# Performance work log

Measured on AMD Instinct MI355X. Metric: run time of the kernel, lower is better.

Reference implementation:

```python
import jax, jax.numpy as jnp
import numpy as np

MARGIN = 1.0


def setup_inputs() -> dict:
    key = jax.random.key(0)
    k1, k2, k3 = jax.random.split(key, 3)
    N, F = 4096, 512
    a = jax.random.normal(k1, (N, F), dtype=jnp.float32)
    b = jax.random.normal(k2, (N, F), dtype=jnp.float32)
    labels = jax.random.randint(k3, (N,), 0, 16, dtype=jnp.int32)
    return {"a": a, "b": b, "labels": labels}


def reference(a, b, labels):
    # D[i, j] = ||b_i - a_j||  (torch: Xa=a[None], Xb=b[:,None], sum over feat)
    # GEMM form of the pairwise sqdist; clamp tiny fp negatives before sqrt.
    Dsq = (jnp.sum(b * b, axis=1)[:, None]
           + jnp.sum(a * a, axis=1)[None, :]
           - 2.0 * (b @ a.T))
    D = jnp.sqrt(jnp.maximum(Dsq, 0.0))            # [N, N]
    Dexpm = jnp.exp(MARGIN - D)                    # [N, N]

    same = labels[:, None] == labels[None, :]      # [N, N]
    eye = jnp.eye(labels.shape[0], dtype=bool)
    pos_mask = same & ~eye                         # ordered positive pairs (i, j)
    neg_mask = ~same                               # negative pairs (labels differ)

    # neg_i sum for row i: sum_k Dexpm[i, k] over k with labels[k] != labels[i]
    row_negsum = jnp.sum(jnp.where(neg_mask, Dexpm, 0.0), axis=1)  # [N]

    # J_ij = log(neg_ik_sum + neg_jl_sum) + D[i, j]; hinged and squared
    J = jnp.log(row_negsum[:, None] + row_negsum[None, :]) + D
    hinge_sq = jnp.square(jnp.maximum(J, 0.0))

    num_pos = jnp.sum(pos_mask)
    return jnp.sum(jnp.where(pos_mask, hinge_sq, 0.0)) / (2.0 * num_pos)
```

## Files before the change

### kernel.cpp

```cpp
#include <hip/hip_runtime.h>
#include <math.h>

#define NROW 4096
#define FDIM 512
#define MARGIN 1.0f
#define NLAB 16
#define PREP_BLK 1024

typedef __attribute__((ext_vector_type(8))) short short8;
typedef __attribute__((ext_vector_type(4))) float floatx4;

__device__ inline unsigned short f2bf(float x) {
    unsigned u = __float_as_uint(x);
    return (unsigned short)((u + 0x7FFFu + ((u >> 16) & 1u)) >> 16);
}
__device__ inline void glds16(const unsigned short* g, unsigned short* l) {
    __builtin_amdgcn_global_load_lds(
        (const __attribute__((address_space(1))) unsigned int*)g,
        (__attribute__((address_space(3))) unsigned int*)l, 16, 0, 0);
}
#define WAIT_VM_BARRIER(N)                                          \
    do {                                                            \
        asm volatile("s_waitcnt vmcnt(" #N ")" ::: "memory");       \
        __builtin_amdgcn_s_barrier();                               \
        __builtin_amdgcn_sched_barrier(0);                          \
    } while (0)

__device__ inline float fast_sqrt_pos(float dsq) {
    float c = fmaxf(dsq, 1e-20f);
    return c * __frsqrt_rn(c);
}

__global__ __launch_bounds__(256) void prep_kernel(
    const float* __restrict__ a, const float* __restrict__ b,
    const int* __restrict__ labels,
    unsigned short* __restrict__ abf, unsigned short* __restrict__ bbf,
    float* __restrict__ na, float* __restrict__ nb,
    float* __restrict__ rns, float* __restrict__ loss,
    int* __restrict__ perm, int* __restrict__ goff,
    int* __restrict__ wl, int* __restrict__ wlmeta) {
    const int t = threadIdx.x;

    if (blockIdx.x == PREP_BLK) {
        __shared__ int hist[NLAB], off[NLAB], cur[NLAB];
        if (t < NLAB) hist[t] = 0;
        __syncthreads();
        for (int i = t; i < NROW; i += 256) atomicAdd(&hist[labels[i] & 15], 1);
        __syncthreads();
        if (t == 0) {
            int acc = 0;
            for (int g = 0; g < NLAB; ++g) { off[g] = acc; acc += hist[g]; }
            int n = 0;
            long long np = 0;
            for (int g = 0; g < NLAB; ++g) {
                goff[g] = off[g];
                int c = hist[g];
                np += (long long)c * (long long)(c - 1);
                int nt = (c + 63) >> 6;
                for (int ti = 0; ti < nt; ++ti)
                    for (int tj = 0; tj < nt; ++tj)
                        wl[n++] = (g << 12) | (ti << 6) | tj;
            }
            goff[NLAB] = NROW;
            wlmeta[0] = n;
            wlmeta[1] = (int)np;
            wlmeta[2] = 0;
            loss[0]   = 0.f;
        }
        __syncthreads();
        if (t < NLAB) cur[t] = off[t];
        __syncthreads();
        for (int i = t; i < NROW; i += 256) {
            int pos = atomicAdd(&cur[labels[i] & 15], 1);
            perm[pos] = i;
        }
        return;
    }

    const int grp = t >> 6;
    const int ln  = t & 63;
    const int row = blockIdx.x * 4 + grp;
    const float4* a4 = (const float4*)(a + (size_t)row * FDIM);
    const float4* b4 = (const float4*)(b + (size_t)row * FDIM);
    const int f = ln * 2;
    float4 va0 = a4[f], va1 = a4[f + 1];
    float4 vb0 = b4[f], vb1 = b4[f + 1];
    float sa = va0.x * va0.x + va0.y * va0.y + va0.z * va0.z + va0.w * va0.w
             + va1.x * va1.x + va1.y * va1.y + va1.z * va1.z + va1.w * va1.w;
    float sb = vb0.x * vb0.x + vb0.y * vb0.y + vb0.z * vb0.z + vb0.w * vb0.w
             + vb1.x * vb1.x + vb1.y * vb1.y + vb1.z * vb1.z + vb1.w * vb1.w;
    short8 ua, ub;
    ua[0] = (short)f2bf(va0.x); ua[1] = (short)f2bf(va0.y);
    ua[2] = (short)f2bf(va0.z); ua[3] = (short)f2bf(va0.w);
    ua[4] = (short)f2bf(va1.x); ua[5] = (short)f2bf(va1.y);
    ua[6] = (short)f2bf(va1.z); ua[7] = (short)f2bf(va1.w);
    ub[0] = (short)f2bf(vb0.x); ub[1] = (short)f2bf(vb0.y);
    ub[2] = (short)f2bf(vb0.z); ub[3] = (short)f2bf(vb0.w);
    ub[4] = (short)f2bf(vb1.x); ub[5] = (short)f2bf(vb1.y);
    ub[6] = (short)f2bf(vb1.z); ub[7] = (short)f2bf(vb1.w);
    *(short8*)&abf[(size_t)row * FDIM + (size_t)f * 4] = ua;
    *(short8*)&bbf[(size_t)row * FDIM + (size_t)f * 4] = ub;
    #pragma unroll
    for (int o = 32; o > 0; o >>= 1) {
        sa += __shfl_down(sa, o);
        sb += __shfl_down(sb, o);
    }
    if (ln == 0) {
        na[row] = sa;
        nb[row] = sb;
        rns[row] = 0.f;
    }
}

__global__ __launch_bounds__(1024, 4) void pass_neg(
    const unsigned short* __restrict__ abf, const unsigned short* __restrict__ bbf,
    const int* __restrict__ labels,
    const float* __restrict__ na, const float* __restrict__ nb,
    float* __restrict__ rns)
{
    __shared__ __align__(16) unsigned short arena[65536];
    __shared__ float rpart[4][256];

    const int t    = threadIdx.x;
    const int lane = t & 63;
    const int w    = t >> 6;
    const int wi   = w >> 2;
    const int wj   = w & 3;
    const int lr   = lane & 15;
    const int lq   = lane >> 4;

    const int bid = blockIdx.x;
    const int wg  = (bid & 7) * 32 + (bid >> 3);
    const int by  = wg >> 4, bx = wg & 15;
    const int ti  = by * 256;
    const int tj  = bx * 256;

    floatx4 acc[4][4];
    #pragma unroll
    for (int i = 0; i < 4; ++i)
        #pragma unroll
        for (int j = 0; j < 4; ++j)
            acc[i][j] = (floatx4){0.f, 0.f, 0.f, 0.f};

    const int srow = t >> 2;
    const int sqs  = (t & 3) ^ ((srow >> 1) & 3);
    const unsigned offA = (unsigned)(tj + srow) * FDIM + sqs * 8;
    const unsigned offB = (unsigned)(ti + srow) * FDIM + sqs * 8;

    auto stage = [&](int s) {
        unsigned short* As = arena + (s & 3) * 16384;
        unsigned short* Bs = As + 8192;
        const int kk = s * 32;
        glds16(abf + offA + kk, As + t * 8);
        glds16(bbf + offB + kk, Bs + t * 8);
    };

    stage(0);
    stage(1);
    stage(2);
    WAIT_VM_BARRIER(4);

    #pragma unroll
    for (int it = 0; it < 16; ++it) {
        if (it < 13) stage(it + 3);

        const unsigned short* As = arena + (it & 3) * 16384;
        const unsigned short* Bs = As + 8192;
        short8 af[4], bv[4];
        #pragma unroll
        for (int ri = 0; ri < 4; ++ri) {
            int R = wi * 64 + ri * 16 + lr;
            af[ri] = *(const short8*)
                &Bs[R * 32 + ((lq ^ ((R >> 1) & 3))) * 8];
        }
        #pragma unroll
        for (int rj = 0; rj < 4; ++rj) {
            int R = wj * 64 + rj * 16 + lr;
            bv[rj] = *(const short8*)
                &As[R * 32 + ((lq ^ ((R >> 1) & 3))) * 8];
        }
        __builtin_amdgcn_s_setprio(1);
        #pragma unroll
        for (int ri = 0; ri < 4; ++ri)
            #pragma unroll
            for (int rj = 0; rj < 4; ++rj)
                acc[ri][rj] = __builtin_amdgcn_mfma_f32_16x16x32_bf16(
                    af[ri], bv[rj], acc[ri][rj], 0, 0, 0);
        __builtin_amdgcn_s_setprio(0);

        if (it < 13) {
            WAIT_VM_BARRIER(4);
        } else if (it == 13) {
            WAIT_VM_BARRIER(2);
        } else if (it == 14) {
            WAIT_VM_BARRIER(0);
        }
    }

    int   ljv[4]; float najv[4];
    #pragma unroll
    for (int rj = 0; rj < 4; ++rj) {
        int jl = wj * 64 + rj * 16 + lr;
        ljv[rj]  = labels[tj + jl];
        najv[rj] = na[tj + jl];
    }
    #pragma unroll
    for (int ri = 0; ri < 4; ++ri) {
        float rs[4] = {0.f, 0.f, 0.f, 0.f};
        int liv[4]; float nbv[4];
        #pragma unroll
        for (int r = 0; r < 4; ++r) {
            int il = wi * 64 + ri * 16 + lq * 4 + r;
            liv[r] = labels[ti + il];
            nbv[r] = nb[ti + il];
        }
        #pragma unroll
        for (int rj = 0; rj < 4; ++rj)
            #pragma unroll
            for (int r = 0; r < 4; ++r) {
                float dsq  = nbv[r] + najv[rj] - 2.f * acc[ri][rj][r];
                float D    = fast_sqrt_pos(dsq);
                float mask = (liv[r] != ljv[rj]) ? 1.f : 0.f;
                rs[r] = fmaf(mask, __expf(MARGIN - D), rs[r]);
            }
        #pragma unroll
        for (int r = 0; r < 4; ++r) {
            #pragma unroll
            for (int o = 8; o > 0; o >>= 1) rs[r] += __shfl_down(rs[r], o, 16);
        }
        if (lr == 0) {
            #pragma unroll
            for (int r = 0; r < 4; ++r)
                rpart[wj][wi * 64 + ri * 16 + lq * 4 + r] = rs[r];
        }
    }
    __syncthreads();
    if (t < 256) {
        float s = rpart[0][t] + rpart[1][t] + rpart[2][t] + rpart[3][t];
        atomicAdd(&rns[ti + t], s);
    }
}

__global__ __launch_bounds__(512) void pass2_pos(
    const unsigned short* __restrict__ abf, const unsigned short* __restrict__ bbf,
    const float* __restrict__ na, const float* __restrict__ nb,
    const float* __restrict__ rns,
    const int* __restrict__ perm, const int* __restrict__ goff,
    const int* __restrict__ wl, const int* __restrict__ wlmeta,
    float* __restrict__ loss_sum, int* __restrict__ done,
    float* __restrict__ out)
{
    __shared__ __align__(16) unsigned short arena[65536];
    __shared__ int   rows_i[64], rows_j[64];
    __shared__ float rbi_s[64], rbj_s[64], nbi_s[64], naj_s[64];
    __shared__ float part[8];

    const int t    = threadIdx.x;
    const int lane = t & 63;
    const int w    = t >> 6;
    const int wi   = w >> 2;
    const int wj   = w & 3;
    const int lr   = lane & 15;
    const int lq   = lane >> 4;
    const int nwl  = wlmeta[0];

    float local = 0.f;

    for (int item = blockIdx.x; item < nwl; item += gridDim.x) {
        __syncthreads();
        int e  = wl[item];
        int g  = e >> 12, ti = (e >> 6) & 63, tj = e & 63;
        int gb = goff[g], ge = goff[g + 1];
        int cnt = ge - gb;

        if (t < 64) {
            int idx = gb + ti * 64 + t;
            int ig  = perm[idx < ge ? idx : gb];
            rows_i[t] = ig;
            rbi_s[t]  = rns[ig];
            nbi_s[t]  = nb[ig];
        } else if (t < 128) {
            int u   = t - 64;
            int idx = gb + tj * 64 + u;
            int jg  = perm[idx < ge ? idx : gb];
            rows_j[u] = jg;
            rbj_s[u]  = rns[jg];
            naj_s[u]  = na[jg];
        }
        __syncthreads();

        #pragma unroll
        for (int l = 0; l < 8; ++l) {
            int c   = t + l * 512;
            int row = c >> 6;
            int qs  = (c & 63) ^ (row & 7);
            glds16(abf + (size_t)rows_j[row] * FDIM + qs * 8, arena + c * 8);
            glds16(bbf + (size_t)rows_i[row] * FDIM + qs * 8,
                   arena + 32768 + c * 8);
        }
        WAIT_VM_BARRIER(0);

        floatx4 acc[2];
        acc[0] = (floatx4){0.f, 0.f, 0.f, 0.f};
        acc[1] = (floatx4){0.f, 0.f, 0.f, 0.f};

        const unsigned short* As = arena;
        const unsigned short* Bs = arena + 32768;
        #pragma unroll
        for (int ks = 0; ks < 16; ++ks) {
            short8 af[2], bv;
            #pragma unroll
            for (int ri = 0; ri < 2; ++ri) {
                int R  = wi * 32 + ri * 16 + lr;
                int cs = (ks * 4 + lq) ^ (R & 7);
                af[ri] = *(const short8*)&Bs[R * 512 + cs * 8];
            }
            {
                int R  = wj * 16 + lr;
                int cs = (ks * 4 + lq) ^ (R & 7);
                bv = *(const short8*)&As[R * 512 + cs * 8];
            }
            #pragma unroll
            for (int ri = 0; ri < 2; ++ri)
                acc[ri] = __builtin_amdgcn_mfma_f32_16x16x32_bf16(
                    af[ri], bv, acc[ri], 0, 0, 0);
        }

        int  jl  = wj * 16 + lr;
        bool vj  = (tj * 64 + jl) < cnt;
        int  jg  = rows_j[jl];
        float nav = naj_s[jl], rbj = rbj_s[jl];
        #pragma unroll
        for (int ri = 0; ri < 2; ++ri) {
            #pragma unroll
            for (int r = 0; r < 4; ++r) {
                int  il = wi * 32 + ri * 16 + lq * 4 + r;
                bool vi = (ti * 64 + il) < cnt;
                if (vi && vj && rows_i[il] != jg) {
                    float dsq = nbi_s[il] + nav - 2.f * acc[ri][r];
                    float D   = fast_sqrt_pos(dsq);
                    float J   = __logf(rbi_s[il] + rbj) + D;
                    float h   = fmaxf(J, 0.f);
                    local += h * h;
                }
            }
        }
    }

    #pragma unroll
    for (int o = 32; o > 0; o >>= 1) local += __shfl_down(local, o);
    if (lane == 0) part[w] = local;
    __syncthreads();
    if (t == 0) {
        float s = 0.f;
        #pragma unroll
        for (int i = 0; i < 8; ++i) s += part[i];
        atomicAdd(loss_sum, s);
        __threadfence();
        int old = atomicAdd(done, 1);
        if (old == (int)gridDim.x - 1) {
            __threadfence();
            float total = *(volatile float*)loss_sum;
            out[0] = total / (2.0f * (float)wlmeta[1]);
        }
    }
}

extern "C" void kernel_launch(void* const* d_in, const int* in_sizes, int n_in,
                              void* d_out, int out_size, void* d_ws, size_t ws_size,
                              hipStream_t stream) {
    const float* a      = (const float*)d_in[0];
    const float* b      = (const float*)d_in[1];
    const int*   labels = (const int*)d_in[2];
    float* out = (float*)d_out;

    unsigned short* abf = (unsigned short*)d_ws;
    unsigned short* bbf = abf + (size_t)NROW * FDIM;
    float* fws  = (float*)(bbf + (size_t)NROW * FDIM);
    float* na   = fws;
    float* nb   = fws + NROW;
    float* rns  = fws + 2 * NROW;
    float* loss = fws + 3 * NROW;
    int* iws    = (int*)(fws + 3 * NROW + 4);
    int* perm   = iws;
    int* goff   = iws + NROW;
    int* wlmeta = iws + NROW + 20;
    int* wl     = iws + NROW + 24;

    prep_kernel<<<PREP_BLK + 1, 256, 0, stream>>>(a, b, labels, abf, bbf,
                                                  na, nb, rns, loss,
                                                  perm, goff, wl, wlmeta);
    pass_neg<<<(NROW / 256) * (NROW / 256), 1024, 0, stream>>>(abf, bbf, labels,
                                                               na, nb, rns);
    pass2_pos<<<256, 512, 0, stream>>>(abf, bbf, na, nb, rns, perm, goff, wl,
                                       wlmeta, loss, &wlmeta[2], out);
}
```

Measured before the change: 123.0 us.

## Sort rows by label and reuse pass_neg distances for positive pairs

Rows are permuted by label before bf16 conversion, so same-label pairs fall into a few diagonal-band 256x256 tiles of the negative pass. Those tiles store D as fp16 in a workspace, and the positive pass becomes an elementwise reduction over the stored values, with no second GEMM. This removes the positive-pair GEMM and its gather loads. In exchange it adds a serial single-block sort kernel before prep, scattered fp16 stores inside pass_neg, and fp16 rounding of D.

After: 144.5 us. 1.17x slower.

```diff
diff --git a/kernel.cpp b/kernel.cpp
--- a/kernel.cpp
+++ b/kernel.cpp
@@ -5,7 +5,7 @@
 #define FDIM 512
 #define MARGIN 1.0f
 #define NLAB 16
-#define PREP_BLK 1024
+#define MAXSLOT 160
 
 typedef __attribute__((ext_vector_type(8))) short short8;
 typedef __attribute__((ext_vector_type(4))) float floatx4;
@@ -13,6 +13,12 @@
 __device__ inline unsigned short f2bf(float x) {
     unsigned u = __float_as_uint(x);
     return (unsigned short)((u + 0x7FFFu + ((u >> 16) & 1u)) >> 16);
+}
+__device__ inline unsigned short f2h(float f) {
+    _Float16 h = (_Float16)f; unsigned short u; __builtin_memcpy(&u, &h, 2); return u;
+}
+__device__ inline float h2f(unsigned short u) {
+    _Float16 h; __builtin_memcpy(&h, &u, 2); return (float)h;
 }
 __device__ inline void glds16(const unsigned short* g, unsigned short* l) {
     __builtin_amdgcn_global_load_lds(
@@ -31,57 +37,67 @@
     return c * __frsqrt_rn(c);
 }
 
+__global__ __launch_bounds__(256) void sort_kernel(
+    const int* __restrict__ labels,
+    int* __restrict__ perm, int* __restrict__ goff, int* __restrict__ labs,
+    int* __restrict__ dslot, int* __restrict__ meta, int* __restrict__ entries,
+    float* __restrict__ loss)
+{
+    __shared__ int hist[NLAB], off[NLAB], cur[NLAB];
+    const int t = threadIdx.x;
+    if (t < NLAB) hist[t] = 0;
+    dslot[t] = -1;
+    __syncthreads();
+    for (int i = t; i < NROW; i += 256) atomicAdd(&hist[labels[i] & 15], 1);
+    __syncthreads();
+    if (t == 0) {
+        int acc = 0;
+        for (int g = 0; g < NLAB; ++g) { off[g] = acc; goff[g] = acc; acc += hist[g]; }
+        goff[NLAB] = NROW;
+        long long np = 0;
+        int ns = 0, ne = 0;
+        for (int g = 0; g < NLAB; ++g) {
+            int c = hist[g];
+            np += (long long)c * (long long)(c - 1);
+            if (c <= 0) continue;
+            int tlo = off[g] >> 8, thi = (off[g] + c - 1) >> 8;
+            for (int by = tlo; by <= thi; ++by)
+                for (int bx = tlo; bx <= thi; ++bx) {
+                    int id = by * 16 + bx;
+                    if (dslot[id] < 0) dslot[id] = ns++;
+                    entries[ne++] = g | (by << 4) | (bx << 8) | (dslot[id] << 12);
+                }
+        }
+        meta[0] = ne;
+        meta[1] = (int)np;
+        meta[2] = 0;
+        loss[0] = 0.f;
+    }
+    __syncthreads();
+    if (t < NLAB) cur[t] = off[t];
+    __syncthreads();
+    for (int i = t; i < NROW; i += 256) {
+        int pos = atomicAdd(&cur[labels[i] & 15], 1);
+        perm[pos] = i;
+    }
+    __syncthreads();
+    for (int i = t; i < NROW; i += 256) labs[i] = labels[perm[i]];
+}
+
 __global__ __launch_bounds__(256) void prep_kernel(
     const float* __restrict__ a, const float* __restrict__ b,
-    const int* __restrict__ labels,
+    const int* __restrict__ perm,
     unsigned short* __restrict__ abf, unsigned short* __restrict__ bbf,
     float* __restrict__ na, float* __restrict__ nb,
-    float* __restrict__ rns, float* __restrict__ loss,
-    int* __restrict__ perm, int* __restrict__ goff,
-    int* __restrict__ wl, int* __restrict__ wlmeta) {
-    const int t = threadIdx.x;
-
-    if (blockIdx.x == PREP_BLK) {
-        __shared__ int hist[NLAB], off[NLAB], cur[NLAB];
-        if (t < NLAB) hist[t] = 0;
-        __syncthreads();
-        for (int i = t; i < NROW; i += 256) atomicAdd(&hist[labels[i] & 15], 1);
-        __syncthreads();
-        if (t == 0) {
-            int acc = 0;
-            for (int g = 0; g < NLAB; ++g) { off[g] = acc; acc += hist[g]; }
-            int n = 0;
-            long long np = 0;
-            for (int g = 0; g < NLAB; ++g) {
-                goff[g] = off[g];
-                int c = hist[g];
-                np += (long long)c * (long long)(c - 1);
-                int nt = (c + 63) >> 6;
-                for (int ti = 0; ti < nt; ++ti)
-                    for (int tj = 0; tj < nt; ++tj)
-                        wl[n++] = (g << 12) | (ti << 6) | tj;
-            }
-            goff[NLAB] = NROW;
-            wlmeta[0] = n;
-            wlmeta[1] = (int)np;
-            wlmeta[2] = 0;
-            loss[0]   = 0.f;
-        }
-        __syncthreads();
-        if (t < NLAB) cur[t] = off[t];
-        __syncthreads();
-        for (int i = t; i < NROW; i += 256) {
-            int pos = atomicAdd(&cur[labels[i] & 15], 1);
-            perm[pos] = i;
-        }
-        return;
-    }
-
+    float* __restrict__ rns)
+{
+    const int t   = threadIdx.x;
     const int grp = t >> 6;
     const int ln  = t & 63;
     const int row = blockIdx.x * 4 + grp;
-    const float4* a4 = (const float4*)(a + (size_t)row * FDIM);
-    const float4* b4 = (const float4*)(b + (size_t)row * FDIM);
+    const int src = perm[row];
+    const float4* a4 = (const float4*)(a + (size_t)src * FDIM);
+    const float4* b4 = (const float4*)(b + (size_t)src * FDIM);
     const int f = ln * 2;
     float4 va0 = a4[f], va1 = a4[f + 1];
     float4 vb0 = b4[f], vb1 = b4[f + 1];
@@ -114,9 +130,10 @@
 
 __global__ __launch_bounds__(1024, 4) void pass_neg(
     const unsigned short* __restrict__ abf, const unsigned short* __restrict__ bbf,
-    const int* __restrict__ labels,
+    const int* __restrict__ labs,
     const float* __restrict__ na, const float* __restrict__ nb,
-    float* __restrict__ rns)
+    float* __restrict__ rns,
+    const int* __restrict__ dslot, unsigned short* __restrict__ dws)
 {
     __shared__ __align__(16) unsigned short arena[65536];
     __shared__ float rpart[4][256];
@@ -134,6 +151,8 @@
     const int by  = wg >> 4, bx = wg & 15;
     const int ti  = by * 256;
     const int tj  = bx * 256;
+    const int sl  = dslot[by * 16 + bx];
+    unsigned short* dblk = dws + (size_t)(sl < 0 ? 0 : sl) * 65536;
 
     floatx4 acc[4][4];
     #pragma unroll
@@ -201,7 +220,7 @@
     #pragma unroll
     for (int rj = 0; rj < 4; ++rj) {
         int jl = wj * 64 + rj * 16 + lr;
-        ljv[rj]  = labels[tj + jl];
+        ljv[rj]  = labs[tj + jl];
         najv[rj] = na[tj + jl];
     }
     #pragma unroll
@@ -211,15 +230,19 @@
         #pragma unroll
         for (int r = 0; r < 4; ++r) {
             int il = wi * 64 + ri * 16 + lq * 4 + r;
-            liv[r] = labels[ti + il];
+            liv[r] = labs[ti + il];
             nbv[r] = nb[ti + il];
         }
         #pragma unroll
         for (int rj = 0; rj < 4; ++rj)
             #pragma unroll
             for (int r = 0; r < 4; ++r) {
+                int il = wi * 64 + ri * 16 + lq * 4 + r;
+                int jl = wj * 64 + rj * 16 + lr;
                 float dsq  = nbv[r] + najv[rj] - 2.f * acc[ri][rj][r];
                 float D    = fast_sqrt_pos(dsq);
+                if (sl >= 0)
+                    dblk[il * 256 + jl] = f2h(D);
                 float mask = (liv[r] != ljv[rj]) ? 1.f : 0.f;
                 rs[r] = fmaf(mask, __expf(MARGIN - D), rs[r]);
             }
@@ -241,127 +264,57 @@
     }
 }
 
-__global__ __launch_bounds__(512) void pass2_pos(
-    const unsigned short* __restrict__ abf, const unsigned short* __restrict__ bbf,
-    const float* __restrict__ na, const float* __restrict__ nb,
-    const float* __restrict__ rns,
-    const int* __restrict__ perm, const int* __restrict__ goff,
-    const int* __restrict__ wl, const int* __restrict__ wlmeta,
-    float* __restrict__ loss_sum, int* __restrict__ done,
-    float* __restrict__ out)
+__global__ __launch_bounds__(256) void pos_kernel(
+    const unsigned short* __restrict__ dws, const float* __restrict__ rns,
+    const int* __restrict__ goff, int* __restrict__ meta,
+    const int* __restrict__ entries,
+    float* __restrict__ loss_sum, float* __restrict__ out)
 {
-    __shared__ __align__(16) unsigned short arena[65536];
-    __shared__ int   rows_i[64], rows_j[64];
-    __shared__ float rbi_s[64], rbj_s[64], nbi_s[64], naj_s[64];
-    __shared__ float part[8];
-
     const int t    = threadIdx.x;
     const int lane = t & 63;
     const int w    = t >> 6;
-    const int wi   = w >> 2;
-    const int wj   = w & 3;
-    const int lr   = lane & 15;
-    const int lq   = lane >> 4;
-    const int nwl  = wlmeta[0];
+    const int ne   = meta[0];
+    const int total = ne << 14;
 
     float local = 0.f;
-
-    for (int item = blockIdx.x; item < nwl; item += gridDim.x) {
-        __syncthreads();
-        int e  = wl[item];
-        int g  = e >> 12, ti = (e >> 6) & 63, tj = e & 63;
-        int gb = goff[g], ge = goff[g + 1];
-        int cnt = ge - gb;
-
-        if (t < 64) {
-            int idx = gb + ti * 64 + t;
-            int ig  = perm[idx < ge ? idx : gb];
-            rows_i[t] = ig;
-            rbi_s[t]  = rns[ig];
-            nbi_s[t]  = nb[ig];
-        } else if (t < 128) {
-            int u   = t - 64;
-            int idx = gb + tj * 64 + u;
-            int jg  = perm[idx < ge ? idx : gb];
-            rows_j[u] = jg;
-            rbj_s[u]  = rns[jg];
-            naj_s[u]  = na[jg];
-        }
-        __syncthreads();
-
-        #pragma unroll
-        for (int l = 0; l < 8; ++l) {
-            int c   = t + l * 512;
-            int row = c >> 6;
-            int qs  = (c & 63) ^ (row & 7);
-            glds16(abf + (size_t)rows_j[row] * FDIM + qs * 8, arena + c * 8);
-            glds16(bbf + (size_t)rows_i[row] * FDIM + qs * 8,
-                   arena + 32768 + c * 8);
-        }
-        WAIT_VM_BARRIER(0);
-
-        floatx4 acc[2];
-        acc[0] = (floatx4){0.f, 0.f, 0.f, 0.f};
-        acc[1] = (floatx4){0.f, 0.f, 0.f, 0.f};
-
-        const unsigned short* As = arena;
-        const unsigned short* Bs = arena + 32768;
-        #pragma unroll
-        for (int ks = 0; ks < 16; ++ks) {
-            short8 af[2], bv;
-            #pragma unroll
-            for (int ri = 0; ri < 2; ++ri) {
-                int R  = wi * 32 + ri * 16 + lr;
-                int cs = (ks * 4 + lq) ^ (R & 7);
-                af[ri] = *(const short8*)&Bs[R * 512 + cs * 8];
+    for (int u = blockIdx.x * 256 + t; u < total; u += gridDim.x * 256) {
+        int e   = entries[u >> 14];
+        int rem = u & 16383;
+        int il  = rem >> 6, jq = rem & 63;
+        int g   = e & 15, by = (e >> 4) & 15, bx = (e >> 8) & 15, sl = e >> 12;
+        int glo = goff[g], ghi = goff[g + 1];
+        int i   = by * 256 + il;
+        if (i < glo || i >= ghi) continue;
+        int j0  = bx * 256 + jq * 4;
+        ushort4 dv = *(const ushort4*)&dws[(size_t)sl * 65536 + il * 256 + jq * 4];
+        float4  rv = *(const float4*)&rns[j0];
+        float   ri_ = rns[i];
+        unsigned short du[4] = {dv.x, dv.y, dv.z, dv.w};
+        float rj_[4] = {rv.x, rv.y, rv.z, rv.w};
+        #pragma unroll
+        for (int k = 0; k < 4; ++k) {
+            int j = j0 + k;
+            if (j >= glo && j < ghi && j != i) {
+                float J = __logf(ri_ + rj_[k]) + h2f(du[k]);
+                float h = fmaxf(J, 0.f);
+                local += h * h;
             }
-            {
-                int R  = wj * 16 + lr;
-                int cs = (ks * 4 + lq) ^ (R & 7);
-                bv = *(const short8*)&As[R * 512 + cs * 8];
-            }
-            #pragma unroll
-            for (int ri = 0; ri < 2; ++ri)
-                acc[ri] = __builtin_amdgcn_mfma_f32_16x16x32_bf16(
-                    af[ri], bv, acc[ri], 0, 0, 0);
-        }
-
-        int  jl  = wj * 16 + lr;
-        bool vj  = (tj * 64 + jl) < cnt;
-        int  jg  = rows_j[jl];
-        float nav = naj_s[jl], rbj = rbj_s[jl];
-        #pragma unroll
-        for (int ri = 0; ri < 2; ++ri) {
-            #pragma unroll
-            for (int r = 0; r < 4; ++r) {
-                int  il = wi * 32 + ri * 16 + lq * 4 + r;
-                bool vi = (ti * 64 + il) < cnt;
-                if (vi && vj && rows_i[il] != jg) {
-                    float dsq = nbi_s[il] + nav - 2.f * acc[ri][r];
-                    float D   = fast_sqrt_pos(dsq);
-                    float J   = __logf(rbi_s[il] + rbj) + D;
-                    float h   = fmaxf(J, 0.f);
-                    local += h * h;
-                }
-            }
-        }
-    }
-
+        }
+    }
+
+    __shared__ float part[4];
     #pragma unroll
     for (int o = 32; o > 0; o >>= 1) local += __shfl_down(local, o);
     if (lane == 0) part[w] = local;
     __syncthreads();
     if (t == 0) {
-        float s = 0.f;
-        #pragma unroll
-        for (int i = 0; i < 8; ++i) s += part[i];
-        atomicAdd(loss_sum, s);
+        atomicAdd(loss_sum, part[0] + part[1] + part[2] + part[3]);
         __threadfence();
-        int old = atomicAdd(done, 1);
+        int old = atomicAdd(&meta[2], 1);
         if (old == (int)gridDim.x - 1) {
             __threadfence();
-            float total = *(volatile float*)loss_sum;
-            out[0] = total / (2.0f * (float)wlmeta[1]);
+            float tot = *(volatile float*)loss_sum;
+            out[0] = tot / (2.0f * (float)meta[1]);
         }
     }
 }
@@ -381,17 +334,22 @@
     float* nb   = fws + NROW;
     float* rns  = fws + 2 * NROW;
     float* loss = fws + 3 * NROW;
-    int* iws    = (int*)(fws + 3 * NROW + 4);
-    int* perm   = iws;
-    int* goff   = iws + NROW;
-    int* wlmeta = iws + NROW + 20;
-    int* wl     = iws + NROW + 24;
-
-    prep_kernel<<<PREP_BLK + 1, 256, 0, stream>>>(a, b, labels, abf, bbf,
-                                                  na, nb, rns, loss,
-                                                  perm, goff, wl, wlmeta);
-    pass_neg<<<(NROW / 256) * (NROW / 256), 1024, 0, stream>>>(abf, bbf, labels,
-                                                               na, nb, rns);
-    pass2_pos<<<256, 512, 0, stream>>>(abf, bbf, na, nb, rns, perm, goff, wl,
-                                       wlmeta, loss, &wlmeta[2], out);
-}
+    int* iws     = (int*)(fws + 3 * NROW + 4);
+    int* perm    = iws;
+    int* goff    = iws + NROW;
+    int* labs    = iws + NROW + 32;
+    int* dslot   = iws + 2 * NROW + 32;
+    int* meta    = iws + 2 * NROW + 288;
+    int* entries = iws + 2 * NROW + 296;
+    unsigned short* dws = (unsigned short*)
+        ((char*)(iws + 2 * NROW + 512) + 16);
+
+    sort_kernel<<<1, 256, 0, stream>>>(labels, perm, goff, labs, dslot,
+                                       meta, entries, loss);
+    prep_kernel<<<NROW / 4, 256, 0, stream>>>(a, b, perm, abf, bbf,
+                                              na, nb, rns);
+    pass_neg<<<(NROW / 256) * (NROW / 256), 1024, 0, stream>>>(
+        abf, bbf, labs, na, nb, rns, dslot, dws);
+    pos_kernel<<<1024, 256, 0, stream>>>(dws, rns, goff, meta, entries,
+                                         loss, out);
+}
```

## Shrink pass_neg tiles to 128x128 with double buffering and supertile rasterization

Applied to the files above, without the earlier changes.

Replaces the 256x256 tile with 1024 threads and a 4-stage async-LDS pipeline by 128x128 tiles using 256 threads, two LDS buffers and a __syncthreads per k-step. Blocks are ordered in 8x8 supertiles, and labels and norms are staged in shared memory. The per-block cross-wave reduction is dropped in favour of direct atomicAdds per row from each wave. This gives 1024 blocks instead of 256, which should help occupancy and load balance on the many CUs. In exchange it doubles global reloads of the operands, adds more barrier stalls, and issues more atomics.

After: 130.9 us. +6.4%, slower.

```diff
diff --git a/kernel.cpp b/kernel.cpp
--- a/kernel.cpp
+++ b/kernel.cpp
@@ -112,28 +112,29 @@
     }
 }
 
-__global__ __launch_bounds__(1024, 4) void pass_neg(
+__global__ __launch_bounds__(256) void pass_neg(
     const unsigned short* __restrict__ abf, const unsigned short* __restrict__ bbf,
     const int* __restrict__ labels,
     const float* __restrict__ na, const float* __restrict__ nb,
     float* __restrict__ rns)
 {
-    __shared__ __align__(16) unsigned short arena[65536];
-    __shared__ float rpart[4][256];
+    __shared__ __align__(16) unsigned short arena[16384];
+    __shared__ int   li_s[128], lj_s[128];
+    __shared__ float nb_s[128], na_s[128];
 
     const int t    = threadIdx.x;
     const int lane = t & 63;
     const int w    = t >> 6;
-    const int wi   = w >> 2;
-    const int wj   = w & 3;
+    const int wi   = w >> 1, wj = w & 1;
+    const int bid  = blockIdx.x;
+    const int sup  = bid >> 6, loc = bid & 63;
+    const int by   = ((sup >> 2) << 3) | (loc >> 3);
+    const int bx   = ((sup & 3) << 3) | (loc & 7);
+    const int ti   = by * 128;
+    const int tj   = bx * 128;
     const int lr   = lane & 15;
     const int lq   = lane >> 4;
-
-    const int bid = blockIdx.x;
-    const int wg  = (bid & 7) * 32 + (bid >> 3);
-    const int by  = wg >> 4, bx = wg & 15;
-    const int ti  = by * 256;
-    const int tj  = bx * 256;
+    const int qe   = lq ^ ((lr >> 1) & 3);
 
     floatx4 acc[4][4];
     #pragma unroll
@@ -142,102 +143,81 @@
         for (int j = 0; j < 4; ++j)
             acc[i][j] = (floatx4){0.f, 0.f, 0.f, 0.f};
 
-    const int srow = t >> 2;
-    const int sqs  = (t & 3) ^ ((srow >> 1) & 3);
-    const unsigned offA = (unsigned)(tj + srow) * FDIM + sqs * 8;
-    const unsigned offB = (unsigned)(ti + srow) * FDIM + sqs * 8;
-
-    auto stage = [&](int s) {
-        unsigned short* As = arena + (s & 3) * 16384;
-        unsigned short* Bs = As + 8192;
-        const int kk = s * 32;
-        glds16(abf + offA + kk, As + t * 8);
-        glds16(bbf + offB + kk, Bs + t * 8);
+    if (t < 128) {
+        li_s[t] = labels[ti + t];
+        nb_s[t] = nb[ti + t];
+    } else {
+        int u = t - 128;
+        lj_s[u] = labels[tj + u];
+        na_s[u] = na[tj + u];
+    }
+
+    auto stage = [&](int kk, int buf) {
+        unsigned short* As = arena + buf * 8192;
+        unsigned short* Bs = arena + 4096 + buf * 8192;
+        #pragma unroll
+        for (int l = 0; l < 2; ++l) {
+            int c   = t + l * 256;
+            int row = c >> 2;
+            int q   = c & 3;
+            int qs  = q ^ ((row >> 1) & 3);
+            glds16(abf + (size_t)(tj + row) * FDIM + kk + qs * 8, As + c * 8);
+            glds16(bbf + (size_t)(ti + row) * FDIM + kk + qs * 8, Bs + c * 8);
+        }
     };
 
-    stage(0);
-    stage(1);
-    stage(2);
-    WAIT_VM_BARRIER(4);
-
-    #pragma unroll
-    for (int it = 0; it < 16; ++it) {
-        if (it < 13) stage(it + 3);
-
-        const unsigned short* As = arena + (it & 3) * 16384;
-        const unsigned short* Bs = As + 8192;
-        short8 af[4], bv[4];
-        #pragma unroll
-        for (int ri = 0; ri < 4; ++ri) {
-            int R = wi * 64 + ri * 16 + lr;
-            af[ri] = *(const short8*)
-                &Bs[R * 32 + ((lq ^ ((R >> 1) & 3))) * 8];
-        }
-        #pragma unroll
-        for (int rj = 0; rj < 4; ++rj) {
-            int R = wj * 64 + rj * 16 + lr;
-            bv[rj] = *(const short8*)
-                &As[R * 32 + ((lq ^ ((R >> 1) & 3))) * 8];
-        }
-        __builtin_amdgcn_s_setprio(1);
+    stage(0, 0);
+    __syncthreads();
+
+    #pragma unroll
+    for (int it = 0; it < FDIM / 32; ++it) {
+        if (it < FDIM / 32 - 1) stage((it + 1) * 32, (it + 1) & 1);
+
+        const unsigned short* As = arena + (it & 1) * 8192;
+        const unsigned short* Bs = As + 4096;
+        short8 af[4], bf[4];
+        #pragma unroll
+        for (int ri = 0; ri < 4; ++ri)
+            af[ri] = *(const short8*)&Bs[(wi * 64 + ri * 16 + lr) * 32 + qe * 8];
+        #pragma unroll
+        for (int rj = 0; rj < 4; ++rj)
+            bf[rj] = *(const short8*)&As[(wj * 64 + rj * 16 + lr) * 32 + qe * 8];
         #pragma unroll
         for (int ri = 0; ri < 4; ++ri)
             #pragma unroll
             for (int rj = 0; rj < 4; ++rj)
                 acc[ri][rj] = __builtin_amdgcn_mfma_f32_16x16x32_bf16(
-                    af[ri], bv[rj], acc[ri][rj], 0, 0, 0);
-        __builtin_amdgcn_s_setprio(0);
-
-        if (it < 13) {
-            WAIT_VM_BARRIER(4);
-        } else if (it == 13) {
-            WAIT_VM_BARRIER(2);
-        } else if (it == 14) {
-            WAIT_VM_BARRIER(0);
-        }
-    }
-
-    int   ljv[4]; float najv[4];
-    #pragma unroll
-    for (int rj = 0; rj < 4; ++rj) {
-        int jl = wj * 64 + rj * 16 + lr;
-        ljv[rj]  = labels[tj + jl];
-        najv[rj] = na[tj + jl];
-    }
+                    af[ri], bf[rj], acc[ri][rj], 0, 0, 0);
+        __syncthreads();
+    }
+
     #pragma unroll
     for (int ri = 0; ri < 4; ++ri) {
         float rs[4] = {0.f, 0.f, 0.f, 0.f};
-        int liv[4]; float nbv[4];
+        #pragma unroll
+        for (int rj = 0; rj < 4; ++rj) {
+            int   jl  = wj * 64 + rj * 16 + lr;
+            float naj = na_s[jl];
+            int   ljv = lj_s[jl];
+            #pragma unroll
+            for (int r = 0; r < 4; ++r) {
+                int il = wi * 64 + ri * 16 + lq * 4 + r;
+                float dsq  = nb_s[il] + naj - 2.f * acc[ri][rj][r];
+                float D    = fast_sqrt_pos(dsq);
+                float mask = (li_s[il] != ljv) ? 1.f : 0.f;
+                rs[r] = fmaf(mask, __expf(MARGIN - D), rs[r]);
+            }
+        }
         #pragma unroll
         for (int r = 0; r < 4; ++r) {
-            int il = wi * 64 + ri * 16 + lq * 4 + r;
-            liv[r] = labels[ti + il];
-            nbv[r] = nb[ti + il];
-        }
-        #pragma unroll
-        for (int rj = 0; rj < 4; ++rj)
-            #pragma unroll
-            for (int r = 0; r < 4; ++r) {
-                float dsq  = nbv[r] + najv[rj] - 2.f * acc[ri][rj][r];
-                float D    = fast_sqrt_pos(dsq);
-                float mask = (liv[r] != ljv[rj]) ? 1.f : 0.f;
-                rs[r] = fmaf(mask, __expf(MARGIN - D), rs[r]);
-            }
-        #pragma unroll
-        for (int r = 0; r < 4; ++r) {
             #pragma unroll
             for (int o = 8; o > 0; o >>= 1) rs[r] += __shfl_down(rs[r], o, 16);
         }
         if (lr == 0) {
             #pragma unroll
             for (int r = 0; r < 4; ++r)
-                rpart[wj][wi * 64 + ri * 16 + lq * 4 + r] = rs[r];
-        }
-    }
-    __syncthreads();
-    if (t < 256) {
-        float s = rpart[0][t] + rpart[1][t] + rpart[2][t] + rpart[3][t];
-        atomicAdd(&rns[ti + t], s);
+                atomicAdd(&rns[ti + wi * 64 + ri * 16 + lq * 4 + r], rs[r]);
+        }
     }
 }
 
@@ -390,8 +370,8 @@
     prep_kernel<<<PREP_BLK + 1, 256, 0, stream>>>(a, b, labels, abf, bbf,
                                                   na, nb, rns, loss,
                                                   perm, goff, wl, wlmeta);
-    pass_neg<<<(NROW / 256) * (NROW / 256), 1024, 0, stream>>>(abf, bbf, labels,
-                                                               na, nb, rns);
+    pass_neg<<<(NROW / 128) * (NROW / 128), 256, 0, stream>>>(abf, bbf, labels,
+                                                              na, nb, rns);
     pass2_pos<<<256, 512, 0, stream>>>(abf, bbf, na, nb, rns, perm, goff, wl,
                                        wlmeta, loss, &wlmeta[2], out);
 }
```
